# Kernel optimization log

Hardware: AMD Instinct MI355X
Metric: run time of the kernel (lower is better)

Reference implementation:

```python
import jax, jax.numpy as jnp
import numpy as np

N_NODES = 100000
N_EDGES = 3200000
IN_FEATS = 16
OUT_FEATS = 2
K = 3


def setup_inputs() -> dict:
    key = jax.random.key(0)
    k1, k2, k3, k4 = jax.random.split(key, 4)
    in_feat = jax.random.normal(k1, (N_NODES, IN_FEATS), dtype=jnp.float32)
    # Linear(K*in_feats -> out_feats, bias=False) weight, torch layout (out, in)
    W = jax.random.normal(k2, (OUT_FEATS, K * IN_FEATS), dtype=jnp.float32) * (1.0 / np.sqrt(K * IN_FEATS))
    src = jax.random.randint(k3, (N_EDGES,), 0, N_NODES, dtype=jnp.int64)
    dst = jax.random.randint(k4, (N_EDGES,), 0, N_NODES, dtype=jnp.int64)
    # cached dgl.laplacian_lambda_max value; 2.0 is the normalized-Laplacian bound
    lambda_max = jnp.full((1,), 2.0, dtype=jnp.float32)
    return {"in_feat": in_feat, "W": W, "src": src, "dst": dst, "lambda_max": lambda_max}


def reference(in_feat, W, src, dst, lambda_max):
    N = in_feat.shape[0]
    # in-degree based symmetric normalization, clamp(min=1)
    deg = jax.ops.segment_sum(jnp.ones_like(dst, dtype=in_feat.dtype), dst, num_segments=N)
    norm = jnp.clip(deg, 1.0) ** -0.5  # (N,)
    norm = norm[:, None]
    re_norm = (2.0 / lambda_max)[None, :]  # (1,1), broadcasts over nodes

    def prop(x):
        # D^{-1/2} A D^{-1/2} x via gather from src, scatter-sum to dst
        m = (x * norm)[src]                                    # (E, d)
        return jax.ops.segment_sum(m, dst, num_segments=N) * norm

    X0 = in_feat
    X1 = -re_norm * prop(X0) + X0 * (re_norm - 1.0)
    X2 = -2.0 * re_norm * prop(X1) + X1 * (2.0 * (re_norm - 1.0)) - X0
    Xt = jnp.concatenate([X0, X1, X2], axis=1)                 # (N, K*d)
    h = Xt @ W.T                                               # (N, out)
    return jax.nn.relu(h)  # DGL ChebConv default activation
```

## Files before the change

kernel.cpp:

```cpp
#include <hip/hip_runtime.h>
#include <hip/hip_bf16.h>


#define NN   100000
#define NE   3200000
#define F    16
#define CB   128
#define NBUK 782
#define ECHK 8192
#define NBLK 391
#define LCAP 5120

__device__ __forceinline__ float bflo(unsigned int u) {
    return __uint_as_float(u << 16);
}
__device__ __forceinline__ float bfhi(unsigned int u) {
    return __uint_as_float(u & 0xffff0000u);
}
__device__ __forceinline__ unsigned int f2bf(float f) {
    __hip_bfloat16 b = __float2bfloat16(f);
    return (unsigned int)*reinterpret_cast<unsigned short*>(&b);
}

__global__ void k_hist(const int* __restrict__ dst, int* __restrict__ H) {
    __shared__ int h[NBUK];
    for (int j = threadIdx.x; j < NBUK; j += 256) h[j] = 0;
    __syncthreads();
    int s0 = blockIdx.x * ECHK;
    int lim = min(s0 + ECHK, NE);
    for (int e = s0 + (int)threadIdx.x; e < lim; e += 256)
        atomicAdd(&h[dst[e] >> 7], 1);
    __syncthreads();
    for (int j = threadIdx.x; j < NBUK; j += 256)
        H[blockIdx.x * NBUK + j] = h[j];
}

__global__ void k_colscan(int* __restrict__ H, int* __restrict__ T) {
    __shared__ int tmp[512];
    int b = blockIdx.x, t = threadIdx.x;
    int v = (t < NBLK) ? H[t * NBUK + b] : 0;
    tmp[t] = v;
    __syncthreads();
    for (int o = 1; o < 512; o <<= 1) {
        int add = (t >= o) ? tmp[t - o] : 0;
        __syncthreads();
        tmp[t] += add;
        __syncthreads();
    }
    if (t < NBLK) H[t * NBUK + b] = tmp[t] - v;
    if (t == 0) T[b] = tmp[511];
}

__global__ void k_basescan(const int* __restrict__ T, int* __restrict__ base) {
    __shared__ int tmp[1024];
    int t = threadIdx.x;
    int v = (t < NBUK) ? T[t] : 0;
    tmp[t] = v;
    __syncthreads();
    for (int o = 1; o < 1024; o <<= 1) {
        int add = (t >= o) ? tmp[t - o] : 0;
        __syncthreads();
        tmp[t] += add;
        __syncthreads();
    }
    if (t < NBUK) base[t] = tmp[t] - v;
    if (t == 0) base[NBUK] = tmp[1023];
}

__global__ __launch_bounds__(512) void k_lsort(const int* __restrict__ src,
        const int* __restrict__ dst, const int* __restrict__ H,
        const int* __restrict__ base, int* __restrict__ packed) {
    __shared__ int pk[ECHK];
    __shared__ int hx[1025];
    __shared__ int cur[1024];
    __shared__ int csum[512];
    int t = threadIdx.x, blk = blockIdx.x;
    for (int j = t; j < 1024; j += 512) hx[j] = 0;
    __syncthreads();
    int s0 = blk * ECHK;
    int lim = min(s0 + ECHK, NE);
    for (int e = s0 + t; e < lim; e += 512)
        atomicAdd(&hx[dst[e] >> 7], 1);
    __syncthreads();
    int b0 = t * 2;
    int c0 = hx[b0], c1 = hx[b0 + 1];
    csum[t] = c0 + c1;
    __syncthreads();
    for (int o = 1; o < 512; o <<= 1) {
        int add = (t >= o) ? csum[t - o] : 0;
        __syncthreads();
        csum[t] += add;
        __syncthreads();
    }
    int ce = csum[t] - (c0 + c1);
    hx[b0] = ce;  hx[b0 + 1] = ce + c0;
    cur[b0] = ce; cur[b0 + 1] = ce + c0;
    if (t == 511) hx[1024] = csum[511];
    __syncthreads();
    for (int e = s0 + t; e < lim; e += 512) {
        int d = dst[e];
        int pos = atomicAdd(&cur[d >> 7], 1);
        pk[pos] = (src[e] << 7) | (d & 127);
    }
    __syncthreads();
    for (int j = t; j < NBUK; j += 512)
        cur[j] = base[j] + H[blk * NBUK + j];
    __syncthreads();
    int g = t >> 3, lane = t & 7;
    for (int b = g; b < NBUK; b += 64) {
        int st = hx[b], len = hx[b + 1] - st;
        int gp = cur[b];
        for (int i = lane; i < len; i += 8)
            packed[gp + i] = pk[st + i];
    }
}

__global__ __launch_bounds__(256) void k_sort(int* __restrict__ packed,
        const int* __restrict__ base, const float* __restrict__ X0,
        int* __restrict__ node_off, float* __restrict__ norm,
        unsigned short* __restrict__ Y0) {
    __shared__ int pk[LCAP];
    __shared__ int cnt[CB], loc[CB], cur[CB];
    __shared__ float nvs[CB];
    int b = blockIdx.x, t = threadIdx.x;
    int beg = base[b], end = base[b + 1];
    int len = end - beg;
    if (len > LCAP) len = LCAP;
    if (t < CB) cnt[t] = 0;
    if (b == 0 && t < F) Y0[(size_t)NN * F + t] = 0;
    __syncthreads();
    for (int i = t; i < len; i += 256) {
        int p = packed[beg + i];
        pk[i] = p;
        atomicAdd(&cnt[p & 127], 1);
    }
    __syncthreads();
    if (t < CB) loc[t] = cnt[t];
    __syncthreads();
    for (int o = 1; o < CB; o <<= 1) {
        int add = 0;
        if (t < CB && t >= o) add = loc[t - o];
        __syncthreads();
        if (t < CB) loc[t] += add;
        __syncthreads();
    }
    if (t < CB) {
        int excl = loc[t] - cnt[t];
        loc[t] = excl;
        cur[t] = 0;
        int n = b * CB + t;
        if (n <= NN) node_off[n] = beg + excl;
        if (n < NN) {
            int c = cnt[t];
            float nv = rsqrtf((float)(c < 1 ? 1 : c));
            norm[n] = nv;
            nvs[t] = nv;
        }
    }
    __syncthreads();
    for (int j = t; j < CB * F; j += 256) {
        int dl = j >> 4;
        int n = b * CB + dl;
        if (n < NN) {
            size_t gidx = (size_t)n * F + (j & 15);
            Y0[gidx] = (unsigned short)f2bf(X0[gidx] * nvs[dl]);
        }
    }
    for (int i = t; i < len; i += 256) {
        int p = pk[i];
        int dl = p & 127;
        int pos = beg + loc[dl] + atomicAdd(&cur[dl], 1);
        packed[pos] = p >> 7;
    }
}

__global__ __launch_bounds__(256) void k_prop1(const int* __restrict__ off,
        const int* __restrict__ es, const unsigned short* __restrict__ Y0,
        const float* __restrict__ X0, const float* __restrict__ norm,
        const float* __restrict__ lm, unsigned short* __restrict__ Y1) {
    int tid = blockIdx.x * 256 + threadIdx.x;
    if (tid < 4) ((uint2*)Y1)[(size_t)NN * 4 + tid] = make_uint2(0u, 0u);
    int n = tid >> 2, h = tid & 3;
    if (n >= NN) return;
    int beg = off[n], end = off[n + 1];
    const uint2* Yv = (const uint2*)Y0;
    float a0 = 0.f, a1 = 0.f, a2 = 0.f, a3 = 0.f;
    for (int e0 = beg; e0 < end; e0 += 8) {
        int c = end - e0;
        int iA = (h < c)     ? es[e0 + h]     : NN;
        int iB = (4 + h < c) ? es[e0 + 4 + h] : NN;
#pragma unroll
        for (int j = 0; j < 4; ++j) {
            int s = __shfl(iA, j, 4);
            uint2 u = Yv[(size_t)s * 4 + h];
            a0 += bflo(u.x); a1 += bfhi(u.x);
            a2 += bflo(u.y); a3 += bfhi(u.y);
        }
#pragma unroll
        for (int j = 0; j < 4; ++j) {
            int s = __shfl(iB, j, 4);
            uint2 u = Yv[(size_t)s * 4 + h];
            a0 += bflo(u.x); a1 += bfhi(u.x);
            a2 += bflo(u.y); a3 += bfhi(u.y);
        }
    }
    float r  = 2.0f / lm[0];
    float nv = norm[n];
    float k1 = -r * nv, k2 = r - 1.0f;
    float4 x0 = ((const float4*)X0)[tid];
    float x1a = k1 * a0 + k2 * x0.x;
    float x1b = k1 * a1 + k2 * x0.y;
    float x1c = k1 * a2 + k2 * x0.z;
    float x1d = k1 * a3 + k2 * x0.w;
    uint2 o;
    o.x = f2bf(nv * x1a) | (f2bf(nv * x1b) << 16);
    o.y = f2bf(nv * x1c) | (f2bf(nv * x1d) << 16);
    ((uint2*)Y1)[tid] = o;
}

__global__ __launch_bounds__(256) void k_prop2(const int* __restrict__ off,
        const int* __restrict__ es, const unsigned short* __restrict__ Y1,
        const float* __restrict__ X0, const float* __restrict__ norm,
        const float* __restrict__ lm, const float* __restrict__ W,
        float* __restrict__ out) {
    __shared__ float Ws[96];
    if (threadIdx.x < 96) Ws[threadIdx.x] = W[threadIdx.x];
    __syncthreads();
    int tid = blockIdx.x * 256 + threadIdx.x;
    int n = tid >> 2, h = tid & 3;
    if (n >= NN) return;
    int beg = off[n], end = off[n + 1];
    const uint2* Yv = (const uint2*)Y1;
    float a0 = 0.f, a1 = 0.f, a2 = 0.f, a3 = 0.f;
    for (int e0 = beg; e0 < end; e0 += 8) {
        int c = end - e0;
        int iA = (h < c)     ? es[e0 + h]     : NN;
        int iB = (4 + h < c) ? es[e0 + 4 + h] : NN;
#pragma unroll
        for (int j = 0; j < 4; ++j) {
            int s = __shfl(iA, j, 4);
            uint2 u = Yv[(size_t)s * 4 + h];
            a0 += bflo(u.x); a1 += bfhi(u.x);
            a2 += bflo(u.y); a3 += bfhi(u.y);
        }
#pragma unroll
        for (int j = 0; j < 4; ++j) {
            int s = __shfl(iB, j, 4);
            uint2 u = Yv[(size_t)s * 4 + h];
            a0 += bflo(u.x); a1 += bfhi(u.x);
            a2 += bflo(u.y); a3 += bfhi(u.y);
        }
    }
    float r  = 2.0f / lm[0];
    float nv = norm[n];
    float rn = 1.0f / nv;
    float4 x0 = ((const float4*)X0)[tid];
    uint2 uy = ((const uint2*)Y1)[tid];
    float x1a = bflo(uy.x) * rn, x1b = bfhi(uy.x) * rn;
    float x1c = bflo(uy.y) * rn, x1d = bfhi(uy.y) * rn;
    float c1 = -2.0f * r * nv, c2 = 2.0f * (r - 1.0f);
    float x2a = c1 * a0 + c2 * x1a - x0.x;
    float x2b = c1 * a1 + c2 * x1b - x0.y;
    float x2c = c1 * a2 + c2 * x1c - x0.z;
    float x2d = c1 * a3 + c2 * x1d - x0.w;
    int f0 = 4 * h;
    float t0 = Ws[f0] * x0.x + Ws[f0 + 1] * x0.y + Ws[f0 + 2] * x0.z + Ws[f0 + 3] * x0.w
             + Ws[16 + f0] * x1a + Ws[17 + f0] * x1b + Ws[18 + f0] * x1c + Ws[19 + f0] * x1d
             + Ws[32 + f0] * x2a + Ws[33 + f0] * x2b + Ws[34 + f0] * x2c + Ws[35 + f0] * x2d;
    float t1 = Ws[48 + f0] * x0.x + Ws[49 + f0] * x0.y + Ws[50 + f0] * x0.z + Ws[51 + f0] * x0.w
             + Ws[64 + f0] * x1a + Ws[65 + f0] * x1b + Ws[66 + f0] * x1c + Ws[67 + f0] * x1d
             + Ws[80 + f0] * x2a + Ws[81 + f0] * x2b + Ws[82 + f0] * x2c + Ws[83 + f0] * x2d;
    t0 += __shfl_xor(t0, 2, 4); t0 += __shfl_xor(t0, 1, 4);
    t1 += __shfl_xor(t1, 2, 4); t1 += __shfl_xor(t1, 1, 4);
    if (h == 0) {
        out[(size_t)n * 2 + 0] = fmaxf(t0, 0.f);
        out[(size_t)n * 2 + 1] = fmaxf(t1, 0.f);
    }
}

extern "C" void kernel_launch(void* const* d_in, const int* in_sizes, int n_in,
                              void* d_out, int out_size, void* d_ws, size_t ws_size,
                              hipStream_t stream) {
    const float* X0  = (const float*)d_in[0];
    const float* W   = (const float*)d_in[1];
    const int*   src = (const int*)d_in[2];
    const int*   dst = (const int*)d_in[3];
    const float* lm  = (const float*)d_in[4];
    float* out = (float*)d_out;

    int*   H        = (int*)d_ws;
    int*   T        = H + (size_t)NBLK * NBUK;
    int*   base     = T + NBUK;
    int*   packed   = base + (NBUK + 1);
    int*   node_off = packed + NE;
    float* norm     = (float*)(node_off + (NN + 1));
    unsigned short* Y0 = (unsigned short*)(norm + NN);
    unsigned short* Y1 = Y0 + (size_t)(NN + 1) * F;

    const int gridP = (NN * 4 + 255) / 256;

    k_hist    <<<NBLK, 256, 0, stream>>>(dst, H);
    k_colscan <<<NBUK, 512, 0, stream>>>(H, T);
    k_basescan<<<1, 1024, 0, stream>>>(T, base);
    k_lsort   <<<NBLK, 512, 0, stream>>>(src, dst, H, base, packed);
    k_sort    <<<NBUK, 256, 0, stream>>>(packed, base, X0, node_off, norm, Y0);
    k_prop1   <<<gridP, 256, 0, stream>>>(node_off, packed, Y0, X0, norm, lm, Y1);
    k_prop2   <<<gridP, 256, 0, stream>>>(node_off, packed, Y1, X0, norm, lm, W, out);
}
```

Measured before the change: 191.6 us.

## Merge histogram into local sort and pull bucket runs in bucket-sort kernel

Drops the separate histogram pass by having the local-sort kernel write per-chunk bucket counts and offsets alongside a chunk-sorted edge array. The bucket kernel then gathers its runs from every chunk, instead of the local-sort kernel scattering them to global positions. This removes one full read of dst and changes the scatter into a gather. Each bucket block issues 391 serial per-thread run copies, which may load-balance poorly. The two propagation kernels also prefetch the next group of 8 edge indices to hide index-load latency.

```diff
diff --git a/kernel.cpp b/kernel.cpp
--- a/kernel.cpp
+++ b/kernel.cpp
@@ -10,6 +10,7 @@
 #define ECHK 8192
 #define NBLK 391
 #define LCAP 5120
+#define HXW  1025
 
 __device__ __forceinline__ float bflo(unsigned int u) {
     return __uint_as_float(u << 16);
@@ -22,17 +23,49 @@
     return (unsigned int)*reinterpret_cast<unsigned short*>(&b);
 }
 
-__global__ void k_hist(const int* __restrict__ dst, int* __restrict__ H) {
-    __shared__ int h[NBUK];
-    for (int j = threadIdx.x; j < NBUK; j += 256) h[j] = 0;
-    __syncthreads();
-    int s0 = blockIdx.x * ECHK;
+__global__ __launch_bounds__(512) void k_lsort(const int* __restrict__ src,
+        const int* __restrict__ dst, int* __restrict__ H, int* __restrict__ hxg,
+        int* __restrict__ csort) {
+    __shared__ int pk[ECHK];
+    __shared__ int hx[HXW];
+    __shared__ int cur[1024];
+    __shared__ int csum[512];
+    int t = threadIdx.x, blk = blockIdx.x;
+    for (int j = t; j < 1024; j += 512) hx[j] = 0;
+    __syncthreads();
+    int s0 = blk * ECHK;
     int lim = min(s0 + ECHK, NE);
-    for (int e = s0 + (int)threadIdx.x; e < lim; e += 256)
-        atomicAdd(&h[dst[e] >> 7], 1);
-    __syncthreads();
-    for (int j = threadIdx.x; j < NBUK; j += 256)
-        H[blockIdx.x * NBUK + j] = h[j];
+    for (int e = s0 + t; e < lim; e += 512)
+        atomicAdd(&hx[dst[e] >> 7], 1);
+    __syncthreads();
+    int b0 = t * 2;
+    int c0 = hx[b0], c1 = hx[b0 + 1];
+    if (b0 < NBUK)     H[blk * NBUK + b0]     = c0;
+    if (b0 + 1 < NBUK) H[blk * NBUK + b0 + 1] = c1;
+    csum[t] = c0 + c1;
+    __syncthreads();
+    for (int o = 1; o < 512; o <<= 1) {
+        int add = (t >= o) ? csum[t - o] : 0;
+        __syncthreads();
+        csum[t] += add;
+        __syncthreads();
+    }
+    int ce = csum[t] - (c0 + c1);
+    hx[b0] = ce;  hx[b0 + 1] = ce + c0;
+    cur[b0] = ce; cur[b0 + 1] = ce + c0;
+    if (t == 511) hx[1024] = csum[511];
+    __syncthreads();
+    for (int j = t; j < HXW; j += 512)
+        hxg[blk * HXW + j] = hx[j];
+    for (int e = s0 + t; e < lim; e += 512) {
+        int d = dst[e];
+        int pos = atomicAdd(&cur[d >> 7], 1);
+        pk[pos] = (src[e] << 7) | (d & 127);
+    }
+    __syncthreads();
+    int len = lim - s0;
+    for (int i = t; i < len; i += 512)
+        csort[s0 + i] = pk[i];
 }
 
 __global__ void k_colscan(int* __restrict__ H, int* __restrict__ T) {
@@ -67,58 +100,11 @@
     if (t == 0) base[NBUK] = tmp[1023];
 }
 
-__global__ __launch_bounds__(512) void k_lsort(const int* __restrict__ src,
-        const int* __restrict__ dst, const int* __restrict__ H,
-        const int* __restrict__ base, int* __restrict__ packed) {
-    __shared__ int pk[ECHK];
-    __shared__ int hx[1025];
-    __shared__ int cur[1024];
-    __shared__ int csum[512];
-    int t = threadIdx.x, blk = blockIdx.x;
-    for (int j = t; j < 1024; j += 512) hx[j] = 0;
-    __syncthreads();
-    int s0 = blk * ECHK;
-    int lim = min(s0 + ECHK, NE);
-    for (int e = s0 + t; e < lim; e += 512)
-        atomicAdd(&hx[dst[e] >> 7], 1);
-    __syncthreads();
-    int b0 = t * 2;
-    int c0 = hx[b0], c1 = hx[b0 + 1];
-    csum[t] = c0 + c1;
-    __syncthreads();
-    for (int o = 1; o < 512; o <<= 1) {
-        int add = (t >= o) ? csum[t - o] : 0;
-        __syncthreads();
-        csum[t] += add;
-        __syncthreads();
-    }
-    int ce = csum[t] - (c0 + c1);
-    hx[b0] = ce;  hx[b0 + 1] = ce + c0;
-    cur[b0] = ce; cur[b0 + 1] = ce + c0;
-    if (t == 511) hx[1024] = csum[511];
-    __syncthreads();
-    for (int e = s0 + t; e < lim; e += 512) {
-        int d = dst[e];
-        int pos = atomicAdd(&cur[d >> 7], 1);
-        pk[pos] = (src[e] << 7) | (d & 127);
-    }
-    __syncthreads();
-    for (int j = t; j < NBUK; j += 512)
-        cur[j] = base[j] + H[blk * NBUK + j];
-    __syncthreads();
-    int g = t >> 3, lane = t & 7;
-    for (int b = g; b < NBUK; b += 64) {
-        int st = hx[b], len = hx[b + 1] - st;
-        int gp = cur[b];
-        for (int i = lane; i < len; i += 8)
-            packed[gp + i] = pk[st + i];
-    }
-}
-
-__global__ __launch_bounds__(256) void k_sort(int* __restrict__ packed,
+__global__ __launch_bounds__(256) void k_sort(const int* __restrict__ csort,
+        const int* __restrict__ H, const int* __restrict__ hxg,
         const int* __restrict__ base, const float* __restrict__ X0,
-        int* __restrict__ node_off, float* __restrict__ norm,
-        unsigned short* __restrict__ Y0) {
+        int* __restrict__ es, int* __restrict__ node_off,
+        float* __restrict__ norm, unsigned short* __restrict__ Y0) {
     __shared__ int pk[LCAP];
     __shared__ int cnt[CB], loc[CB], cur[CB];
     __shared__ float nvs[CB];
@@ -129,11 +115,20 @@
     if (t < CB) cnt[t] = 0;
     if (b == 0 && t < F) Y0[(size_t)NN * F + t] = 0;
     __syncthreads();
-    for (int i = t; i < len; i += 256) {
-        int p = packed[beg + i];
-        pk[i] = p;
-        atomicAdd(&cnt[p & 127], 1);
-    }
+    for (int c = t; c < NBLK; c += 256) {
+        int h0 = hxg[c * HXW + b];
+        int h1 = hxg[c * HXW + b + 1];
+        int dpos = H[c * NBUK + b];
+        int rl = h1 - h0;
+        if (dpos >= LCAP) continue;
+        if (dpos + rl > LCAP) rl = LCAP - dpos;
+        int sbase = c * ECHK + h0;
+        for (int i = 0; i < rl; ++i)
+            pk[dpos + i] = csort[sbase + i];
+    }
+    __syncthreads();
+    for (int i = t; i < len; i += 256)
+        atomicAdd(&cnt[pk[i] & 127], 1);
     __syncthreads();
     if (t < CB) loc[t] = cnt[t];
     __syncthreads();
@@ -170,7 +165,7 @@
         int p = pk[i];
         int dl = p & 127;
         int pos = beg + loc[dl] + atomicAdd(&cur[dl], 1);
-        packed[pos] = p >> 7;
+        es[pos] = p >> 7;
     }
 }
 
@@ -185,10 +180,15 @@
     int beg = off[n], end = off[n + 1];
     const uint2* Yv = (const uint2*)Y0;
     float a0 = 0.f, a1 = 0.f, a2 = 0.f, a3 = 0.f;
-    for (int e0 = beg; e0 < end; e0 += 8) {
-        int c = end - e0;
-        int iA = (h < c)     ? es[e0 + h]     : NN;
-        int iB = (4 + h < c) ? es[e0 + 4 + h] : NN;
+    int e0 = beg;
+    int c = end - e0;
+    int iA = (h < c)     ? es[e0 + h]     : NN;
+    int iB = (4 + h < c) ? es[e0 + 4 + h] : NN;
+    while (e0 < end) {
+        int e1 = e0 + 8;
+        int c1 = end - e1;
+        int nA = (h < c1)     ? es[e1 + h]     : NN;
+        int nB = (4 + h < c1) ? es[e1 + 4 + h] : NN;
 #pragma unroll
         for (int j = 0; j < 4; ++j) {
             int s = __shfl(iA, j, 4);
@@ -203,6 +203,7 @@
             a0 += bflo(u.x); a1 += bfhi(u.x);
             a2 += bflo(u.y); a3 += bfhi(u.y);
         }
+        iA = nA; iB = nB; e0 = e1;
     }
     float r  = 2.0f / lm[0];
     float nv = norm[n];
@@ -232,10 +233,15 @@
     int beg = off[n], end = off[n + 1];
     const uint2* Yv = (const uint2*)Y1;
     float a0 = 0.f, a1 = 0.f, a2 = 0.f, a3 = 0.f;
-    for (int e0 = beg; e0 < end; e0 += 8) {
-        int c = end - e0;
-        int iA = (h < c)     ? es[e0 + h]     : NN;
-        int iB = (4 + h < c) ? es[e0 + 4 + h] : NN;
+    int e0 = beg;
+    int c = end - e0;
+    int iA = (h < c)     ? es[e0 + h]     : NN;
+    int iB = (4 + h < c) ? es[e0 + 4 + h] : NN;
+    while (e0 < end) {
+        int e1 = e0 + 8;
+        int c1 = end - e1;
+        int nA = (h < c1)     ? es[e1 + h]     : NN;
+        int nB = (4 + h < c1) ? es[e1 + 4 + h] : NN;
 #pragma unroll
         for (int j = 0; j < 4; ++j) {
             int s = __shfl(iA, j, 4);
@@ -250,6 +256,7 @@
             a0 += bflo(u.x); a1 += bfhi(u.x);
             a2 += bflo(u.y); a3 += bfhi(u.y);
         }
+        iA = nA; iB = nB; e0 = e1;
     }
     float r  = 2.0f / lm[0];
     float nv = norm[n];
@@ -289,21 +296,22 @@
     float* out = (float*)d_out;
 
     int*   H        = (int*)d_ws;
-    int*   T        = H + (size_t)NBLK * NBUK;
+    int*   hxg      = H + (size_t)NBLK * NBUK;
+    int*   T        = hxg + (size_t)NBLK * HXW;
     int*   base     = T + NBUK;
-    int*   packed   = base + (NBUK + 1);
-    int*   node_off = packed + NE;
+    int*   csort    = base + (NBUK + 1);
+    int*   es       = csort + NE;
+    int*   node_off = es + NE;
     float* norm     = (float*)(node_off + (NN + 1));
     unsigned short* Y0 = (unsigned short*)(norm + NN);
     unsigned short* Y1 = Y0 + (size_t)(NN + 1) * F;
 
     const int gridP = (NN * 4 + 255) / 256;
 
-    k_hist    <<<NBLK, 256, 0, stream>>>(dst, H);
+    k_lsort   <<<NBLK, 512, 0, stream>>>(src, dst, H, hxg, csort);
     k_colscan <<<NBUK, 512, 0, stream>>>(H, T);
     k_basescan<<<1, 1024, 0, stream>>>(T, base);
-    k_lsort   <<<NBLK, 512, 0, stream>>>(src, dst, H, base, packed);
-    k_sort    <<<NBUK, 256, 0, stream>>>(packed, base, X0, node_off, norm, Y0);
-    k_prop1   <<<gridP, 256, 0, stream>>>(node_off, packed, Y0, X0, norm, lm, Y1);
-    k_prop2   <<<gridP, 256, 0, stream>>>(node_off, packed, Y1, X0, norm, lm, W, out);
-}
+    k_sort    <<<NBUK, 256, 0, stream>>>(csort, H, hxg, base, X0, es, node_off, norm, Y0);
+    k_prop1   <<<gridP, 256, 0, stream>>>(node_off, es, Y0, X0, norm, lm, Y1);
+    k_prop2   <<<gridP, 256, 0, stream>>>(node_off, es, Y1, X0, norm, lm, W, out);
+}
```

New measurement: 196.8 us. 1.03x slower.
